# Kernel optimization log

Measured on AMD Instinct MI355X. Metric: run time of the kernel, lower is better.

The kernel has to match this reference:

```python
import jax, jax.numpy as jnp
import numpy as np

B, S = 32, 256          # batch, sequence
D = 128                 # d_model
I = 256                 # mamba intermediate = 2*D
N = 16                  # ssm state size
R = 8                   # dt rank = ceil(D/16)
K = 4                   # conv kernel
L = 4                   # num mamba layers
Z = 128                 # vib z_dim
FUT = 20                # future steps


def setup_inputs() -> dict:
    key = jax.random.key(0)
    ks = iter(jax.random.split(key, 40))

    def nrm(shape, scale=0.02):
        return jax.random.normal(next(ks), shape, dtype=jnp.float32) * scale

    return {
        "x_cam": jax.random.normal(next(ks), (B, S, 8, 1024), dtype=jnp.float32),
        "x_ego": jax.random.normal(next(ks), (B, S, 64), dtype=jnp.float32),
        "vib_eps": jax.random.normal(next(ks), (B, Z), dtype=jnp.float32),
        "vis_w1": nrm((8 * 1024, 512)), "vis_b1": jnp.zeros((512,), jnp.float32),
        "vis_w2": nrm((512, D)), "vis_b2": jnp.zeros((D,), jnp.float32),
        "ego_w": nrm((64, D)), "ego_b": jnp.zeros((D,), jnp.float32),
        "fus_w": nrm((2 * D, D)), "fus_b": jnp.zeros((D,), jnp.float32),
        "norm_w": jnp.ones((L, D), jnp.float32),
        "in_proj_w": nrm((L, D, 2 * I)),
        "conv_w": nrm((L, I, K), 0.1), "conv_b": jnp.zeros((L, I), jnp.float32),
        "x_proj_w": nrm((L, I, R + 2 * N)),
        "dt_proj_w": nrm((L, R, I), 0.1), "dt_proj_b": jnp.full((L, I), -2.0, jnp.float32),
        "A_log": jnp.tile(jnp.log(jnp.arange(1, N + 1, dtype=jnp.float32))[None, None, :], (L, I, 1)),
        "D_par": jnp.ones((L, I), jnp.float32),
        "out_proj_w": nrm((L, I, D)),
        "normf_w": jnp.ones((D,), jnp.float32),
        "mu_w": nrm((D, Z)), "mu_b": jnp.zeros((Z,), jnp.float32),
        "lv_w": nrm((D, Z)), "lv_b": jnp.zeros((Z,), jnp.float32),
        "h1_w": nrm((Z, 256)), "h1_b": jnp.zeros((256,), jnp.float32),
        "h2_w": nrm((256, FUT * 2)), "h2_b": jnp.zeros((FUT * 2,), jnp.float32),
    }


def _rms(x, w, eps=1e-5):
    return x * jax.lax.rsqrt(jnp.mean(x * x, axis=-1, keepdims=True) + eps) * w


def _mixer(x, inw, cw, cb, xpw, dtw, dtb, alog, dpar, outw):
    # x: [B,S,D]
    Bb, Ss, _ = x.shape
    h, gate = jnp.split(x @ inw, 2, axis=-1)            # [B,S,I] each
    # depthwise causal conv (kernel K)
    hp = jnp.pad(h, ((0, 0), (K - 1, 0), (0, 0)))
    h = sum(hp[:, k:k + Ss, :] * cw[:, k] for k in range(K)) + cb
    h = jax.nn.silu(h)
    ssm = h @ xpw                                        # [B,S,R+2N]
    dt = jax.nn.softplus(ssm[..., :R] @ dtw + dtb)       # [B,S,I]
    Bm = ssm[..., R:R + N]                               # [B,S,N]
    Cm = ssm[..., R + N:]                                # [B,S,N]
    A = -jnp.exp(alog)                                   # [I,N]
    dA = jnp.exp(dt[..., None] * A)                      # [B,S,I,N]
    dBu = dt[..., None] * Bm[:, :, None, :] * h[..., None]  # [B,S,I,N]

    def step(carry, t):
        dA_t, dBu_t, C_t = t
        carry = carry * dA_t + dBu_t                     # [B,I,N]
        return carry, jnp.einsum('bin,bn->bi', carry, C_t)

    h0 = jnp.zeros((Bb, I, N), dtype=x.dtype)
    _, ys = jax.lax.scan(step, h0, (dA.swapaxes(0, 1), dBu.swapaxes(0, 1), Cm.swapaxes(0, 1)))
    y = ys.swapaxes(0, 1) + h * dpar                     # [B,S,I]
    y = y * jax.nn.silu(gate)
    return y @ outw                                      # [B,S,D]


def _mamba(x, norm_w, in_proj_w, conv_w, conv_b, x_proj_w, dt_proj_w, dt_proj_b, A_log, D_par, out_proj_w, normf_w):
    for l in range(L):
        x = x + _mixer(_rms(x, norm_w[l]), in_proj_w[l], conv_w[l], conv_b[l],
                       x_proj_w[l], dt_proj_w[l], dt_proj_b[l], A_log[l], D_par[l], out_proj_w[l])
    return _rms(x, normf_w)


def _forward(x_cam, x_ego, vib_eps, vis_w1, vis_b1, vis_w2, vis_b2, ego_w, ego_b, fus_w, fus_b,
             norm_w, in_proj_w, conv_w, conv_b, x_proj_w, dt_proj_w, dt_proj_b, A_log, D_par,
             out_proj_w, normf_w, mu_w, mu_b, lv_w, lv_b, h1_w, h1_b, h2_w, h2_b):
    Bb, Ss = x_cam.shape[:2]
    v = x_cam.reshape(Bb, Ss, -1)                                          # [B,S,8192]
    v = jax.nn.gelu(v @ vis_w1 + vis_b1, approximate=False) @ vis_w2 + vis_b2
    e = x_ego @ ego_w + ego_b
    fused = jax.nn.gelu(jnp.concatenate([v, e], axis=-1) @ fus_w + fus_b, approximate=False)
    h = _mamba(fused, norm_w, in_proj_w, conv_w, conv_b, x_proj_w,
               dt_proj_w, dt_proj_b, A_log, D_par, out_proj_w, normf_w)
    last = h[:, -1, :]                                                     # [B,D]
    mu = last @ mu_w + mu_b
    logvar = last @ lv_w + lv_b
    z = mu + vib_eps * jnp.exp(0.5 * logvar)
    kl = -0.5 * jnp.mean(1.0 + logvar - mu * mu - jnp.exp(logvar))
    out = jax.nn.relu(z @ h1_w + h1_b) @ h2_w + h2_b
    return out.reshape(Bb, FUT, 2), kl


def reference(x_cam, x_ego, vib_eps, vis_w1, vis_b1, vis_w2, vis_b2, ego_w, ego_b, fus_w, fus_b,
              norm_w, in_proj_w, conv_w, conv_b, x_proj_w, dt_proj_w, dt_proj_b, A_log, D_par,
              out_proj_w, normf_w, mu_w, mu_b, lv_w, lv_b, h1_w, h1_b, h2_w, h2_b):
    return _forward(x_cam, x_ego, vib_eps, vis_w1, vis_b1, vis_w2, vis_b2, ego_w, ego_b, fus_w, fus_b,
                    norm_w, in_proj_w, conv_w, conv_b, x_proj_w, dt_proj_w, dt_proj_b, A_log, D_par,
                    out_proj_w, normf_w, mu_w, mu_b, lv_w, lv_b, h1_w, h1_b, h2_w, h2_b)
```

## Files before the change

### kernel.cpp

```cpp
#include <hip/hip_runtime.h>
#include <hip/hip_bf16.h>
#include <math.h>

#define BQ 32
#define SQ 256
#define MTOK 8192
#define DD 128
#define II 256
#define NNs 16
#define RRs 8
#define KKs 4
#define LLs 4
#define ZZs 128
#define FUTs 20

typedef __attribute__((ext_vector_type(8))) short bf8v;
typedef __attribute__((ext_vector_type(4))) float f4v;

__device__ __forceinline__ float geluf(float x){ return 0.5f*x*(1.0f+erff(x*0.70710678118654752f)); }
__device__ __forceinline__ float siluf(float x){ return x/(1.0f+__expf(-x)); }
__device__ __forceinline__ float softplusf(float x){ return fmaxf(x,0.0f)+log1pf(__expf(-fabsf(x))); }
__device__ __forceinline__ unsigned short f2bf(float x){
    __hip_bfloat16 h = __float2bfloat16(x);
    return *reinterpret_cast<unsigned short*>(&h);
}

__device__ __forceinline__ void gload_lds16(const void* g, void* l){
    __builtin_amdgcn_global_load_lds(
        (const __attribute__((address_space(1))) void*)g,
        (__attribute__((address_space(3))) void*)l, 16, 0, 0);
}

#define PIPE_WAIT_BAR(N) do {                                   \
    __builtin_amdgcn_sched_barrier(0);                          \
    asm volatile("s_waitcnt vmcnt(" #N ")" ::: "memory");       \
    __builtin_amdgcn_s_barrier();                               \
    __builtin_amdgcn_sched_barrier(0);                          \
} while(0)

#define PIPE_END_BAR() do {                                     \
    __builtin_amdgcn_sched_barrier(0);                          \
    asm volatile("s_waitcnt lgkmcnt(0)" ::: "memory");          \
    __builtin_amdgcn_s_barrier();                               \
    __builtin_amdgcn_sched_barrier(0);                          \
} while(0)

template<int ACT,int ADD,int OUTBF>
__launch_bounds__(512,1)
__global__ void gemm_w512_kernel(const unsigned short* __restrict__ A,
                                 const unsigned short* __restrict__ Bt,
                                 const float* __restrict__ bias,
                                 void* __restrict__ Cv,
                                 int M, int N, int Kd, int ldc)
{
    __shared__ __align__(16) unsigned short As[3][128*64];
    __shared__ __align__(16) unsigned short Bs[3][128*64];
    const int tid = threadIdx.x;
    const int w = tid >> 6, lane = tid & 63;
    const int ml = lane & 15, quad = lane >> 4;
    const int wm = w >> 2, wn = w & 3;
    const int rowBase = blockIdx.x * 128, colBase = blockIdx.y * 128;

    const int srow = lane >> 3;
    const int scol = (((lane&7) ^ (lane>>3)))*8;

    f4v acc[4][2];
    #pragma unroll
    for (int i=0;i<4;i++)
      #pragma unroll
      for (int j=0;j<2;j++) acc[i][j] = (f4v){0.f,0.f,0.f,0.f};

    auto stage = [&](int buf, int kt){
        #pragma unroll
        for (int e=0;e<2;e++){
            const int c = w*2 + e;
            const unsigned short* srcA = A + (size_t)(rowBase + c*8 + srow)*Kd + kt + scol;
            gload_lds16(srcA, (unsigned short*)As[buf] + c*512);
            const unsigned short* srcB = Bt + (size_t)(colBase + c*8 + srow)*Kd + kt + scol;
            gload_lds16(srcB, (unsigned short*)Bs[buf] + c*512);
        }
    };

    const int swz = (ml&7)*8;

    auto compute = [&](int buf){
        #pragma unroll
        for (int ks=0; ks<2; ks++){
            const int co = (ks*32 + quad*8) ^ swz;
            bf8v a[4], b[2];
            #pragma unroll
            for (int mf=0; mf<4; mf++)
                a[mf] = *reinterpret_cast<const bf8v*>(&As[buf][(wm*64 + mf*16 + ml)*64 + co]);
            #pragma unroll
            for (int nf=0; nf<2; nf++)
                b[nf] = *reinterpret_cast<const bf8v*>(&Bs[buf][(wn*32 + nf*16 + ml)*64 + co]);
            #pragma unroll
            for (int mf=0; mf<4; mf++)
                #pragma unroll
                for (int nf=0; nf<2; nf++)
                    acc[mf][nf] = __builtin_amdgcn_mfma_f32_16x16x32_bf16(a[mf], b[nf], acc[mf][nf], 0,0,0);
        }
    };

    const int nIter = Kd >> 6;
    stage(0, 0);
    stage(1, 64);

    int i = 0;
    for (; i + 2 < nIter; ++i){
        stage((i+2)%3, (i+2)<<6);
        PIPE_WAIT_BAR(8);
        compute(i%3);
        PIPE_END_BAR();
    }
    PIPE_WAIT_BAR(4);
    compute(i%3);
    PIPE_END_BAR();
    ++i;
    PIPE_WAIT_BAR(0);
    compute(i%3);

    #pragma unroll
    for (int mf=0; mf<4; mf++){
        #pragma unroll
        for (int nf=0; nf<2; nf++){
            int col = colBase + wn*32 + nf*16 + ml;
            float bb = bias ? bias[col] : 0.0f;
            #pragma unroll
            for (int r=0;r<4;r++){
                int row = rowBase + wm*64 + mf*16 + quad*4 + r;
                float v = acc[mf][nf][r] + bb;
                if (ACT==1) v = geluf(v);
                if constexpr (OUTBF==1){
                    ((unsigned short*)Cv)[(size_t)row*ldc + col] = f2bf(v);
                } else {
                    float* cp = (float*)Cv + (size_t)row*ldc + col;
                    if (ADD) v += *cp;
                    *cp = v;
                }
            }
        }
    }
}

template<int ACT,int ADD,int OUTBF>
__launch_bounds__(256,2)
__global__ void gemm_lds64_kernel(const unsigned short* __restrict__ A,
                                  const unsigned short* __restrict__ Bt,
                                  const float* __restrict__ bias,
                                  void* __restrict__ Cv,
                                  int M, int N, int Kd, int ldc)
{
    __shared__ __align__(16) unsigned short As[3][64*64];
    __shared__ __align__(16) unsigned short Bs[3][64*64];
    const int tid = threadIdx.x;
    const int w = tid >> 6, lane = tid & 63;
    const int ml = lane & 15, quad = lane >> 4;
    const int rowBase = blockIdx.x * 64, colBase = blockIdx.y * 64;

    const int srow = lane >> 3;
    const int scol = (((lane&7) ^ (lane>>3)))*8;

    f4v acc[4];
    #pragma unroll
    for (int j=0;j<4;j++) acc[j] = (f4v){0.f,0.f,0.f,0.f};

    auto stage = [&](int buf, int kt){
        #pragma unroll
        for (int e=0;e<2;e++){
            const int c = w*2 + e;
            const unsigned short* srcA = A + (size_t)(rowBase + c*8 + srow)*Kd + kt + scol;
            gload_lds16(srcA, (unsigned short*)As[buf] + c*512);
            const unsigned short* srcB = Bt + (size_t)(colBase + c*8 + srow)*Kd + kt + scol;
            gload_lds16(srcB, (unsigned short*)Bs[buf] + c*512);
        }
    };

    const int swz = (ml&7)*8;

    auto compute = [&](int buf){
        #pragma unroll
        for (int ks=0; ks<2; ks++){
            const int co = (ks*32 + quad*8) ^ swz;
            bf8v a0 = *reinterpret_cast<const bf8v*>(&As[buf][(w*16 + ml)*64 + co]);
            #pragma unroll
            for (int nt=0; nt<4; nt++){
                bf8v b = *reinterpret_cast<const bf8v*>(&Bs[buf][(nt*16+ml)*64 + co]);
                acc[nt] = __builtin_amdgcn_mfma_f32_16x16x32_bf16(a0, b, acc[nt], 0,0,0);
            }
        }
    };

    const int nIter = Kd >> 6;
    stage(0, 0);
    stage(1, 64);

    int i = 0;
    for (; i + 2 < nIter; ++i){
        stage((i+2)%3, (i+2)<<6);
        PIPE_WAIT_BAR(8);
        compute(i%3);
        PIPE_END_BAR();
    }
    PIPE_WAIT_BAR(4);
    compute(i%3);
    PIPE_END_BAR();
    ++i;
    PIPE_WAIT_BAR(0);
    compute(i%3);

    #pragma unroll
    for (int nt=0; nt<4; nt++){
        int col = colBase + nt*16 + ml;
        float bb = bias ? bias[col] : 0.0f;
        #pragma unroll
        for (int r=0;r<4;r++){
            int row = rowBase + w*16 + quad*4 + r;
            float v = acc[nt][r] + bb;
            if (ACT==1) v = geluf(v);
            if constexpr (OUTBF==1){
                ((unsigned short*)Cv)[(size_t)row*ldc + col] = f2bf(v);
            } else {
                float* cp = (float*)Cv + (size_t)row*ldc + col;
                if (ADD) v += *cp;
                *cp = v;
            }
        }
    }
}

template<int ACT,int ADD,int OUTBF,typename AT>
__launch_bounds__(256,2)
__global__ void gemm_bf16_kernel(const AT* __restrict__ A,
                                 const unsigned short* __restrict__ Bt,
                                 const float* __restrict__ bias,
                                 void* __restrict__ Cv,
                                 int M, int N, int Kd, int ldc)
{
    constexpr int LDK = 72;
    __shared__ unsigned short As[128*LDK];
    __shared__ unsigned short Bs[64*LDK];
    const int tid = threadIdx.x;
    const int w = tid >> 6, lane = tid & 63;
    const int ml = lane & 15, quad = lane >> 4;
    const int rowBase = blockIdx.x * 128, colBase = blockIdx.y * 64;

    f4v acc[2][4];
    #pragma unroll
    for (int i=0;i<2;i++)
      #pragma unroll
      for (int j=0;j<4;j++) acc[i][j] = (f4v){0.f,0.f,0.f,0.f};

    bf8v pa[4], pb[2];
    const int ar = tid >> 3, as8 = (tid & 7) * 8;

    auto loadTile = [&](int kt){
        #pragma unroll
        for (int e=0;e<4;e++){
            int r = ar + e*32;
            if constexpr (sizeof(AT)==2){
                pa[e] = *reinterpret_cast<const bf8v*>(
                    (const unsigned short*)A + (size_t)(rowBase+r)*Kd + kt + as8);
            } else {
                const float* ap = (const float*)A + (size_t)(rowBase+r)*Kd + kt + as8;
                float4 v0 = *reinterpret_cast<const float4*>(ap);
                float4 v1 = *reinterpret_cast<const float4*>(ap+4);
                union { unsigned short u[8]; bf8v v; } o;
                o.u[0]=f2bf(v0.x); o.u[1]=f2bf(v0.y); o.u[2]=f2bf(v0.z); o.u[3]=f2bf(v0.w);
                o.u[4]=f2bf(v1.x); o.u[5]=f2bf(v1.y); o.u[6]=f2bf(v1.z); o.u[7]=f2bf(v1.w);
                pa[e] = o.v;
            }
        }
        #pragma unroll
        for (int e=0;e<2;e++){
            int r = ar + e*32;
            pb[e] = *reinterpret_cast<const bf8v*>(
                Bt + (size_t)(colBase+r)*Kd + kt + as8);
        }
    };

    loadTile(0);

    for (int kt=0; kt<Kd; kt+=64){
        #pragma unroll
        for (int e=0;e<4;e++) *reinterpret_cast<bf8v*>(&As[(ar+e*32)*LDK + as8]) = pa[e];
        #pragma unroll
        for (int e=0;e<2;e++) *reinterpret_cast<bf8v*>(&Bs[(ar+e*32)*LDK + as8]) = pb[e];
        __syncthreads();
        if (kt + 64 < Kd) loadTile(kt + 64);
        #pragma unroll
        for (int ks=0; ks<2; ks++){
            bf8v a0 = *reinterpret_cast<bf8v*>(&As[(w*32 +      ml)*LDK + ks*32 + quad*8]);
            bf8v a1 = *reinterpret_cast<bf8v*>(&As[(w*32 + 16 + ml)*LDK + ks*32 + quad*8]);
            #pragma unroll
            for (int nt=0; nt<4; nt++){
                bf8v b = *reinterpret_cast<bf8v*>(&Bs[(nt*16+ml)*LDK + ks*32 + quad*8]);
                acc[0][nt] = __builtin_amdgcn_mfma_f32_16x16x32_bf16(a0, b, acc[0][nt], 0,0,0);
                acc[1][nt] = __builtin_amdgcn_mfma_f32_16x16x32_bf16(a1, b, acc[1][nt], 0,0,0);
            }
        }
        __syncthreads();
    }

    #pragma unroll
    for (int mt=0; mt<2; mt++){
        #pragma unroll
        for (int nt=0; nt<4; nt++){
            int col = colBase + nt*16 + ml;
            float bb = bias ? bias[col] : 0.0f;
            #pragma unroll
            for (int r=0;r<4;r++){
                int row = rowBase + w*32 + mt*16 + quad*4 + r;
                float v = acc[mt][nt][r] + bb;
                if (ACT==1) v = geluf(v);
                if constexpr (OUTBF==1){
                    ((unsigned short*)Cv)[(size_t)row*ldc + col] = f2bf(v);
                } else {
                    float* cp = (float*)Cv + (size_t)row*ldc + col;
                    if (ADD) v += *cp;
                    *cp = v;
                }
            }
        }
    }
}

__launch_bounds__(256)
__global__ void cast_bf16_kernel(const float* __restrict__ in, unsigned short* __restrict__ out)
{
    size_t i = (size_t)blockIdx.x*256 + threadIdx.x;
    const float4 v0 = reinterpret_cast<const float4*>(in)[i*2];
    const float4 v1 = reinterpret_cast<const float4*>(in)[i*2+1];
    union { unsigned short u[8]; bf8v v; } o;
    o.u[0]=f2bf(v0.x); o.u[1]=f2bf(v0.y); o.u[2]=f2bf(v0.z); o.u[3]=f2bf(v0.w);
    o.u[4]=f2bf(v1.x); o.u[5]=f2bf(v1.y); o.u[6]=f2bf(v1.z); o.u[7]=f2bf(v1.w);
    reinterpret_cast<bf8v*>(out)[i] = o.v;
}

__launch_bounds__(256)
__global__ void castT_kernel(const float* __restrict__ in, unsigned short* __restrict__ out,
                             int Kd, int N)
{
    __shared__ float t[64][65];
    int k0 = blockIdx.y*64, n0 = blockIdx.x*64;
    int c = threadIdx.x & 63, r4 = threadIdx.x >> 6;
    #pragma unroll
    for (int it=0; it<16; it++){
        int row = it*4 + r4;
        t[row][c] = in[(size_t)(k0+row)*N + n0 + c];
    }
    __syncthreads();
    #pragma unroll
    for (int it=0; it<16; it++){
        int row = it*4 + r4;
        out[(size_t)(n0+row)*Kd + k0 + c] = f2bf(t[c][row]);
    }
}

__launch_bounds__(256)
__global__ void rms_bf_kernel(const float* __restrict__ x, const float* __restrict__ w,
                              unsigned short* __restrict__ out)
{
    int tid = threadIdx.x;
    int lane = tid & 63, wv = tid >> 6;
    int token = blockIdx.x*4 + wv;
    const float* xr = x + (size_t)token*DD;
    float v0 = xr[lane], v1 = xr[lane+64];
    float ss = v0*v0 + v1*v1;
    #pragma unroll
    for (int off=32; off>0; off>>=1) ss += __shfl_xor(ss, off);
    float r = rsqrtf(ss*(1.0f/DD) + 1e-5f);
    unsigned short* o = out + (size_t)token*DD;
    o[lane]    = f2bf(v0*r*w[lane]);
    o[lane+64] = f2bf(v1*r*w[lane+64]);
}

__launch_bounds__(256)
__global__ void conv_kernel(const float* __restrict__ hg, const float* __restrict__ cw,
                            const float* __restrict__ cb, float* __restrict__ hc)
{
    int idx = blockIdx.x*256 + threadIdx.x;
    int i = idx & (II-1);
    int m = idx >> 8;
    int s = m & (SQ-1);
    const float* w = cw + i*KKs;
    float a = cb[i];
    #pragma unroll
    for (int k=0;k<KKs;k++){
        int ssrc = s + k - (KKs-1);
        if (ssrc >= 0) a += hg[(size_t)(m + k - (KKs-1))*(2*II) + i] * w[k];
    }
    hc[idx] = siluf(a);
}

#define XT 16
__launch_bounds__(256)
__global__ void xproj_fused_kernel(const float* __restrict__ hconv,
                                   const float* __restrict__ xpw,
                                   const float* __restrict__ dtw,
                                   const float* __restrict__ dtb,
                                   float* __restrict__ dt_out,
                                   float* __restrict__ bc)
{
    __shared__ float sh[XT][II+4];
    __shared__ float ssm_s[XT][40];
    const int tid = threadIdx.x;
    const int m0 = blockIdx.x * XT;

    {
        const float4* src = reinterpret_cast<const float4*>(hconv + (size_t)m0*II);
        #pragma unroll
        for (int e=0;e<4;e++){
            int idx = e*256 + tid;
            int t = idx >> 6, c = idx & 63;
            *reinterpret_cast<float4*>(&sh[t][c*4]) = src[idx];
        }
    }
    __syncthreads();

    for (int e = tid; e < XT*40; e += 256){
        int t = e / 40, o = e - t*40;
        float a0=0.f, a1=0.f, a2=0.f, a3=0.f;
        #pragma unroll 16
        for (int k=0;k<II;k+=4){
            float4 h4 = *reinterpret_cast<const float4*>(&sh[t][k]);
            a0 += h4.x*xpw[(k+0)*40+o];
            a1 += h4.y*xpw[(k+1)*40+o];
            a2 += h4.z*xpw[(k+2)*40+o];
            a3 += h4.w*xpw[(k+3)*40+o];
        }
        ssm_s[t][o] = (a0+a1)+(a2+a3);
    }
    __syncthreads();

    #pragma unroll
    for (int e = tid; e < XT*32; e += 256){
        int t = e >> 5, n = e & 31;
        bc[(size_t)(m0+t)*32 + n] = ssm_s[t][8+n];
    }

    {
        const int i = tid;
        float wr[RRs];
        #pragma unroll
        for (int r=0;r<RRs;r++) wr[r] = dtw[r*II + i];
        const float bb = dtb[i];
        #pragma unroll 4
        for (int t=0;t<XT;t++){
            float a = bb;
            #pragma unroll
            for (int r=0;r<RRs;r++) a += ssm_s[t][r]*wr[r];
            dt_out[(size_t)(m0+t)*II + i] = softplusf(a);
        }
    }
}

__launch_bounds__(256)
__global__ void scan_kernel(const float* __restrict__ dtp, const float* __restrict__ bc,
                            const float* __restrict__ hconv, const float* __restrict__ hg,
                            const float* __restrict__ A_log, const float* __restrict__ D_par,
                            unsigned short* __restrict__ ybf)
{
    __shared__ float sdt[16][17], shv[16][17], sgv[16][17], sbc[16][33];
    int b = blockIdx.x >> 4, chunk = blockIdx.x & 15;
    int tid = threadIdx.x;
    int n = tid & 15, il = tid >> 4;
    int i = chunk*16 + il;
    float A2 = -__expf(A_log[i*NNs + n]) * 1.44269504f;
    float carry = 0.0f;
    const float dpi = D_par[i];
    const int m0 = b*SQ;
    const int li = tid & 15, ls = tid >> 4;
    const int gi = chunk*16 + li;
    for (int cs=0; cs<16; cs++){
        __syncthreads();
        int mload = m0 + cs*16 + ls;
        sdt[ls][li] = dtp[(size_t)mload*II + gi];
        shv[ls][li] = hconv[(size_t)mload*II + gi];
        sgv[ls][li] = hg[(size_t)mload*(2*II) + II + gi];
        sbc[ls][li]      = bc[(size_t)mload*32 + li];
        sbc[ls][li + 16] = bc[(size_t)mload*32 + 16 + li];
        __syncthreads();
        #pragma unroll
        for (int s=0; s<16; s++){
            float dtv = sdt[s][il];
            float hv  = shv[s][il];
            float dA  = exp2f(dtv*A2);
            carry = carry*dA + dtv*hv*sbc[s][n];
            float acc = carry*sbc[s][16+n];
            acc += __shfl_xor(acc, 1);
            acc += __shfl_xor(acc, 2);
            acc += __shfl_xor(acc, 4);
            acc += __shfl_xor(acc, 8);
            if (n == 0){
                ybf[(size_t)(m0 + cs*16 + s)*II + i] =
                    f2bf((acc + hv*dpi) * siluf(sgv[s][il]));
            }
        }
    }
}

__launch_bounds__(128)
__global__ void head_kernel(const float* __restrict__ x, const float* __restrict__ normf,
                            const float* __restrict__ mu_w, const float* __restrict__ mu_b,
                            const float* __restrict__ lv_w, const float* __restrict__ lv_b,
                            const float* __restrict__ eps, const float* __restrict__ h1_w,
                            const float* __restrict__ h1_b, const float* __restrict__ h2_w,
                            const float* __restrict__ h2_b, float* __restrict__ out,
                            float* __restrict__ klacc)
{
    __shared__ float lasts[DD];
    __shared__ float zs[DD];
    __shared__ float hr[256];
    __shared__ float red[2];
    int b = blockIdx.x, d = threadIdx.x;
    int lane = d & 63, wv = d >> 6;
    float xv = x[((size_t)(b*SQ + SQ-1))*DD + d];
    float ss = xv*xv;
    #pragma unroll
    for (int off=32; off>0; off>>=1) ss += __shfl_xor(ss, off);
    if (lane==0) red[wv] = ss;
    __syncthreads();
    float tot = red[0] + red[1];
    float last = xv * rsqrtf(tot*(1.0f/DD) + 1e-5f) * normf[d];
    lasts[d] = last;
    __syncthreads();
    float mu = mu_b[d], lv = lv_b[d];
    for (int j=0;j<DD;j++){
        float lj = lasts[j];
        mu += lj*mu_w[j*DD + d];
        lv += lj*lv_w[j*DD + d];
    }
    float z = mu + eps[b*ZZs + d]*__expf(0.5f*lv);
    zs[d] = z;
    float klp = 1.0f + lv - mu*mu - __expf(lv);
    #pragma unroll
    for (int off=32; off>0; off>>=1) klp += __shfl_xor(klp, off);
    if (lane==0) red[wv] = klp;
    __syncthreads();
    if (d==0) atomicAdd(klacc, red[0]+red[1]);
    for (int o=d; o<256; o+=128){
        float a = h1_b[o];
        for (int j=0;j<DD;j++) a += zs[j]*h1_w[j*256 + o];
        hr[o] = fmaxf(a, 0.0f);
    }
    __syncthreads();
    if (d < 40){
        float a = h2_b[d];
        for (int k=0;k<256;k++) a += hr[k]*h2_w[k*40 + d];
        out[b*(FUTs*2) + d] = a;
    }
}

__global__ void kl_final_kernel(const float* __restrict__ klacc, float* __restrict__ out)
{
    out[0] = -0.5f * klacc[0] * (1.0f/(BQ*ZZs));
}

extern "C" void kernel_launch(void* const* d_in, const int* in_sizes, int n_in,
                              void* d_out, int out_size, void* d_ws, size_t ws_size,
                              hipStream_t stream)
{
    const float* x_cam     = (const float*)d_in[0];
    const float* x_ego     = (const float*)d_in[1];
    const float* vib_eps   = (const float*)d_in[2];
    const float* vis_w1    = (const float*)d_in[3];
    const float* vis_b1    = (const float*)d_in[4];
    const float* vis_w2    = (const float*)d_in[5];
    const float* vis_b2    = (const float*)d_in[6];
    const float* ego_w     = (const float*)d_in[7];
    const float* ego_b     = (const float*)d_in[8];
    const float* fus_w     = (const float*)d_in[9];
    const float* fus_b     = (const float*)d_in[10];
    const float* norm_w    = (const float*)d_in[11];
    const float* in_proj_w = (const float*)d_in[12];
    const float* conv_w    = (const float*)d_in[13];
    const float* conv_b    = (const float*)d_in[14];
    const float* x_proj_w  = (const float*)d_in[15];
    const float* dt_proj_w = (const float*)d_in[16];
    const float* dt_proj_b = (const float*)d_in[17];
    const float* A_log     = (const float*)d_in[18];
    const float* D_par     = (const float*)d_in[19];
    const float* out_proj_w= (const float*)d_in[20];
    const float* normf_w   = (const float*)d_in[21];
    const float* mu_w      = (const float*)d_in[22];
    const float* mu_b      = (const float*)d_in[23];
    const float* lv_w      = (const float*)d_in[24];
    const float* lv_b      = (const float*)d_in[25];
    const float* h1_w      = (const float*)d_in[26];
    const float* h1_b      = (const float*)d_in[27];
    const float* h2_w      = (const float*)d_in[28];
    const float* h2_b      = (const float*)d_in[29];

    float* ws = (float*)d_ws;
    float* hg    = ws;
    unsigned short* v1g  = (unsigned short*)hg;
    float* hconv = ws + 4194304;
    unsigned short* catbf = (unsigned short*)hconv;
    float* xbuf  = ws + 6291456;
    float* dtws  = ws + 7340032;
    float* bcws  = ws + 9437184;
    unsigned short* ybf  = (unsigned short*)(ws + 9699328);
    unsigned short* xnbf = (unsigned short*)(ws + 10747904);
    unsigned short* w1t  = (unsigned short*)(ws + 11272192);
    unsigned short* w2t  = (unsigned short*)(ws + 13369344);
    unsigned short* egot = (unsigned short*)(ws + 13402112);
    unsigned short* fust = (unsigned short*)(ws + 13406208);
    unsigned short* wipt = (unsigned short*)(ws + 13422592);
    unsigned short* wopt = (unsigned short*)(ws + 13553664);
    float* klacc = ws + 13619200;
    unsigned short* xcbf = (unsigned short*)(ws + 13619208);
    const size_t need_bytes = (size_t)(13619208 + 33554432) * 4;
    const bool big_ws = (ws_size >= need_bytes);

    hipMemsetAsync(klacc, 0, sizeof(float), stream);

    castT_kernel<<<dim3(8, 128), 256, 0, stream>>>(vis_w1, w1t, 8192, 512);
    castT_kernel<<<dim3(2, 8),   256, 0, stream>>>(vis_w2, w2t, 512, 128);
    castT_kernel<<<dim3(2, 1),   256, 0, stream>>>(ego_w,  egot, 64, 128);
    castT_kernel<<<dim3(2, 4),   256, 0, stream>>>(fus_w,  fust, 256, 128);
    for (int l=0; l<LLs; l++){
        castT_kernel<<<dim3(8, 2), 256, 0, stream>>>(
            in_proj_w + (size_t)l*DD*2*II, wipt + (size_t)l*2*II*DD, DD, 2*II);
        castT_kernel<<<dim3(2, 4), 256, 0, stream>>>(
            out_proj_w + (size_t)l*II*DD, wopt + (size_t)l*DD*II, II, DD);
    }

    if (big_ws){
        cast_bf16_kernel<<<32768, 256, 0, stream>>>(x_cam, xcbf);
        gemm_w512_kernel<1,0,1><<<dim3(64, 4), 512, 0, stream>>>(
            xcbf, w1t, vis_b1, v1g, MTOK, 512, 8192, 512);
    } else {
        gemm_bf16_kernel<1,0,1,float><<<dim3(64, 8), 256, 0, stream>>>(
            x_cam, w1t, vis_b1, v1g, MTOK, 512, 8192, 512);
    }
    gemm_lds64_kernel<0,0,1><<<dim3(128, 2), 256, 0, stream>>>(
        v1g, w2t, vis_b2, catbf, MTOK, 128, 512, 256);
    gemm_bf16_kernel<0,0,1,float><<<dim3(64, 2), 256, 0, stream>>>(
        x_ego, egot, ego_b, catbf + 128, MTOK, 128, 64, 256);
    gemm_lds64_kernel<1,0,0><<<dim3(128, 2), 256, 0, stream>>>(
        catbf, fust, fus_b, xbuf, MTOK, 128, 256, 128);

    for (int l=0; l<LLs; l++){
        rms_bf_kernel<<<MTOK/4, 256, 0, stream>>>(xbuf, norm_w + l*DD, xnbf);
        gemm_w512_kernel<0,0,0><<<dim3(64, 4), 512, 0, stream>>>(
            xnbf, wipt + (size_t)l*2*II*DD, nullptr, hg, MTOK, 2*II, DD, 2*II);
        conv_kernel<<<MTOK*II/256, 256, 0, stream>>>(
            hg, conv_w + (size_t)l*II*KKs, conv_b + (size_t)l*II, hconv);
        xproj_fused_kernel<<<MTOK/XT, 256, 0, stream>>>(
            hconv, x_proj_w + (size_t)l*II*40, dt_proj_w + (size_t)l*RRs*II,
            dt_proj_b + (size_t)l*II, dtws, bcws);
        scan_kernel<<<BQ*16, 256, 0, stream>>>(
            dtws, bcws, hconv, hg, A_log + (size_t)l*II*NNs, D_par + (size_t)l*II, ybf);
        gemm_lds64_kernel<0,1,0><<<dim3(128, 2), 256, 0, stream>>>(
            ybf, wopt + (size_t)l*DD*II, nullptr, xbuf, MTOK, DD, II, DD);
    }

    head_kernel<<<BQ, 128, 0, stream>>>(
        xbuf, normf_w, mu_w, mu_b, lv_w, lv_b, vib_eps,
        h1_w, h1_b, h2_w, h2_b, (float*)d_out, klacc);
    kl_final_kernel<<<1, 1, 0, stream>>>(klacc, (float*)d_out + 1280);
}
```

Measured before the change: 1.228 ms.

## Fuse fp32-to-bf16 cast of camera input into the big visual GEMM

Replaces the separate cast kernel plus bf16 GEMM with one GEMM that loads fp32 A tiles into registers, converts them to bf16 and writes them to swizzled LDS. B is still staged with direct global-to-LDS loads, double-buffered. This removes the 256MB-read/128MB-write cast pass and its intermediate buffer. The trade-off is that the GEMM now reads fp32 A (twice the bytes of bf16), once per column block (4 times), and uses a shallower two-stage pipeline with register-staged A.

```diff
diff --git a/kernel.cpp b/kernel.cpp
--- a/kernel.cpp
+++ b/kernel.cpp
@@ -44,6 +44,121 @@
     __builtin_amdgcn_s_barrier();                               \
     __builtin_amdgcn_sched_barrier(0);                          \
 } while(0)
+
+template<int ACT,int OUTBF>
+__launch_bounds__(512,1)
+__global__ void gemm_f32a_kernel(const float* __restrict__ A,
+                                 const unsigned short* __restrict__ Bt,
+                                 const float* __restrict__ bias,
+                                 void* __restrict__ Cv,
+                                 int M, int N, int Kd, int ldc)
+{
+    __shared__ __align__(16) unsigned short As[2][128*64];
+    __shared__ __align__(16) unsigned short Bs[2][128*64];
+    const int tid = threadIdx.x;
+    const int w = tid >> 6, lane = tid & 63;
+    const int ml = lane & 15, quad = lane >> 4;
+    const int wm = w >> 2, wn = w & 3;
+    const int rowBase = blockIdx.x * 128, colBase = blockIdx.y * 128;
+
+    const int arow  = tid >> 3;
+    const int aslot = tid & 7;
+    const int awslot = aslot ^ (arow & 7);
+
+    const int srow = lane >> 3;
+    const int scol = (((lane&7) ^ (lane>>3)))*8;
+
+    f4v acc[4][2];
+    #pragma unroll
+    for (int i=0;i<4;i++)
+      #pragma unroll
+      for (int j=0;j<2;j++) acc[i][j] = (f4v){0.f,0.f,0.f,0.f};
+
+    float4 pa[2][2];
+    auto loadA = [&](int kt){
+        #pragma unroll
+        for (int c=0;c<2;c++){
+            const float* ap = A + (size_t)(rowBase + arow + c*64)*Kd + kt + aslot*8;
+            pa[c][0] = *reinterpret_cast<const float4*>(ap);
+            pa[c][1] = *reinterpret_cast<const float4*>(ap+4);
+        }
+    };
+    auto writeA = [&](int buf){
+        #pragma unroll
+        for (int c=0;c<2;c++){
+            union { unsigned short u[8]; bf8v v; } o;
+            o.u[0]=f2bf(pa[c][0].x); o.u[1]=f2bf(pa[c][0].y);
+            o.u[2]=f2bf(pa[c][0].z); o.u[3]=f2bf(pa[c][0].w);
+            o.u[4]=f2bf(pa[c][1].x); o.u[5]=f2bf(pa[c][1].y);
+            o.u[6]=f2bf(pa[c][1].z); o.u[7]=f2bf(pa[c][1].w);
+            *reinterpret_cast<bf8v*>(&As[buf][(arow + c*64)*64 + awslot*8]) = o.v;
+        }
+    };
+    auto stageB = [&](int buf, int kt){
+        #pragma unroll
+        for (int e=0;e<2;e++){
+            const int c = w*2 + e;
+            const unsigned short* src = Bt + (size_t)(colBase + c*8 + srow)*Kd + kt + scol;
+            gload_lds16(src, (unsigned short*)Bs[buf] + c*512);
+        }
+    };
+
+    const int swz = (ml&7)*8;
+    auto compute = [&](int buf){
+        #pragma unroll
+        for (int ks=0; ks<2; ks++){
+            const int co = (ks*32 + quad*8) ^ swz;
+            bf8v a[4], b[2];
+            #pragma unroll
+            for (int mf=0; mf<4; mf++)
+                a[mf] = *reinterpret_cast<const bf8v*>(&As[buf][(wm*64 + mf*16 + ml)*64 + co]);
+            #pragma unroll
+            for (int nf=0; nf<2; nf++)
+                b[nf] = *reinterpret_cast<const bf8v*>(&Bs[buf][(wn*32 + nf*16 + ml)*64 + co]);
+            #pragma unroll
+            for (int mf=0; mf<4; mf++)
+                #pragma unroll
+                for (int nf=0; nf<2; nf++)
+                    acc[mf][nf] = __builtin_amdgcn_mfma_f32_16x16x32_bf16(a[mf], b[nf], acc[mf][nf], 0,0,0);
+        }
+    };
+
+    loadA(0);
+    stageB(0, 0);
+    writeA(0);
+    __syncthreads();
+
+    int buf = 0;
+    for (int kt=0; kt<Kd; kt+=64){
+        const bool more = (kt + 64 < Kd);
+        if (more){ loadA(kt+64); stageB(buf^1, kt+64); }
+        compute(buf);
+        if (more) writeA(buf^1);
+        __syncthreads();
+        buf ^= 1;
+    }
+
+    #pragma unroll
+    for (int mf=0; mf<4; mf++){
+        #pragma unroll
+        for (int nf=0; nf<2; nf++){
+            int col = colBase + wn*32 + nf*16 + ml;
+            float bb = bias ? bias[col] : 0.0f;
+            #pragma unroll
+            for (int r=0;r<4;r++){
+                int row = rowBase + wm*64 + mf*16 + quad*4 + r;
+                float v = acc[mf][nf][r] + bb;
+                if (ACT==1) v = geluf(v);
+                if constexpr (OUTBF==1){
+                    ((unsigned short*)Cv)[(size_t)row*ldc + col] = f2bf(v);
+                } else {
+                    float* cp = (float*)Cv + (size_t)row*ldc + col;
+                    *cp = v;
+                }
+            }
+        }
+    }
+}
 
 template<int ACT,int ADD,int OUTBF>
 __launch_bounds__(512,1)
@@ -323,18 +438,6 @@
             }
         }
     }
-}
-
-__launch_bounds__(256)
-__global__ void cast_bf16_kernel(const float* __restrict__ in, unsigned short* __restrict__ out)
-{
-    size_t i = (size_t)blockIdx.x*256 + threadIdx.x;
-    const float4 v0 = reinterpret_cast<const float4*>(in)[i*2];
-    const float4 v1 = reinterpret_cast<const float4*>(in)[i*2+1];
-    union { unsigned short u[8]; bf8v v; } o;
-    o.u[0]=f2bf(v0.x); o.u[1]=f2bf(v0.y); o.u[2]=f2bf(v0.z); o.u[3]=f2bf(v0.w);
-    o.u[4]=f2bf(v1.x); o.u[5]=f2bf(v1.y); o.u[6]=f2bf(v1.z); o.u[7]=f2bf(v1.w);
-    reinterpret_cast<bf8v*>(out)[i] = o.v;
 }
 
 __launch_bounds__(256)
@@ -609,9 +712,6 @@
     unsigned short* wipt = (unsigned short*)(ws + 13422592);
     unsigned short* wopt = (unsigned short*)(ws + 13553664);
     float* klacc = ws + 13619200;
-    unsigned short* xcbf = (unsigned short*)(ws + 13619208);
-    const size_t need_bytes = (size_t)(13619208 + 33554432) * 4;
-    const bool big_ws = (ws_size >= need_bytes);
 
     hipMemsetAsync(klacc, 0, sizeof(float), stream);
 
@@ -626,14 +726,8 @@
             out_proj_w + (size_t)l*II*DD, wopt + (size_t)l*DD*II, II, DD);
     }
 
-    if (big_ws){
-        cast_bf16_kernel<<<32768, 256, 0, stream>>>(x_cam, xcbf);
-        gemm_w512_kernel<1,0,1><<<dim3(64, 4), 512, 0, stream>>>(
-            xcbf, w1t, vis_b1, v1g, MTOK, 512, 8192, 512);
-    } else {
-        gemm_bf16_kernel<1,0,1,float><<<dim3(64, 8), 256, 0, stream>>>(
-            x_cam, w1t, vis_b1, v1g, MTOK, 512, 8192, 512);
-    }
+    gemm_f32a_kernel<1,1><<<dim3(64, 4), 512, 0, stream>>>(
+        x_cam, w1t, vis_b1, v1g, MTOK, 512, 8192, 512);
     gemm_lds64_kernel<0,0,1><<<dim3(128, 2), 256, 0, stream>>>(
         v1g, w2t, vis_b2, catbf, MTOK, 128, 512, 256);
     gemm_bf16_kernel<0,0,1,float><<<dim3(64, 2), 256, 0, stream>>>(
```

Result: faster. 1.173 ms (-4.5%).
